# Kernel optimization log

Measured on AMD Instinct MI355X. Metric: run time of the kernel, lower is better.

## Reference

```python
import jax, jax.numpy as jnp
import numpy as np

B, T, D = 2, 2048, 2048
NH, NKV, HD = 16, 4, 128
EPS = 1e-6
ROPE_THETA = 10000.0


def rms_norm(x, w):
    # per-head RMSNorm over the last (head_dim) axis
    var = jnp.mean(jnp.square(x), axis=-1, keepdims=True)
    return x * jax.lax.rsqrt(var + EPS) * w


def rope_sin_cos(seq_len, dim, dtype):
    inv_freq = 1.0 / (ROPE_THETA ** (jnp.arange(0, dim, 2, dtype=jnp.float32) / dim))
    t = jnp.arange(seq_len, dtype=jnp.float32)
    ang = jnp.outer(t, inv_freq)                      # [T, HD/2]
    ang = jnp.concatenate([ang, ang], axis=-1)         # [T, HD]
    return jnp.sin(ang).astype(dtype), jnp.cos(ang).astype(dtype)


def rotate_half(x):
    x1, x2 = jnp.split(x, 2, axis=-1)
    return jnp.concatenate([-x2, x1], axis=-1)


def apply_rope(x, sin, cos):
    # x: [B, T, H, HD]; sin/cos: [T, HD]
    s = sin[None, :, None, :]
    c = cos[None, :, None, :]
    return x * c + rotate_half(x) * s


def setup_inputs() -> dict:
    key = jax.random.key(0)
    ks = jax.random.split(key, 5)
    scale = 1.0 / np.sqrt(D)
    return {
        "x": jax.random.normal(ks[0], (B, T, D), jnp.float32),
        "wq": jax.random.normal(ks[1], (D, D), jnp.float32) * scale,
        "wk": jax.random.normal(ks[2], (NKV * HD, D), jnp.float32) * scale,
        "wv": jax.random.normal(ks[3], (NKV * HD, D), jnp.float32) * scale,
        "wo": jax.random.normal(ks[4], (D, D), jnp.float32) * scale,
        "q_norm_w": jnp.ones((HD,), jnp.float32),
        "k_norm_w": jnp.ones((HD,), jnp.float32),
    }


def reference(x, wq, wk, wv, wo, q_norm_w, k_norm_w):
    b, t, _ = x.shape
    q = (x @ wq.T).reshape(b, t, NH, HD)    # [B,T,NH,HD]
    k = (x @ wk.T).reshape(b, t, NKV, HD)   # [B,T,NKV,HD]
    v = (x @ wv.T).reshape(b, t, NKV, HD)

    # per-head QK RMS norm
    q = rms_norm(q, q_norm_w)
    k = rms_norm(k, k_norm_w)

    # RoPE
    sin, cos = rope_sin_cos(t, HD, x.dtype)
    q = apply_rope(q, sin, cos)
    k = apply_rope(k, sin, cos)

    # GQA: expand kv heads to match query heads
    rep = NH // NKV
    k = jnp.repeat(k, rep, axis=2)          # [B,T,NH,HD]
    v = jnp.repeat(v, rep, axis=2)

    # causal SDPA
    scale = 1.0 / np.sqrt(HD)
    scores = jnp.einsum('bqhd,bkhd->bhqk', q, k) * scale
    causal = jnp.tril(jnp.ones((t, t), bool))
    scores = jnp.where(causal[None, None], scores, jnp.finfo(scores.dtype).min)
    probs = jax.nn.softmax(scores, axis=-1)
    att = jnp.einsum('bhqk,bkhd->bqhd', probs, v).reshape(b, t, NH * HD)
    return att @ wo.T
```

## Files before the change

kernel.cpp:

```cpp
#include <hip/hip_runtime.h>
#include <hip/hip_bf16.h>

#define B_ 2
#define T_ 2048
#define D_ 2048
#define NH_ 16
#define NKV_ 4
#define HD_ 128

using bf16 = __bf16;
using bf16x8 = __attribute__((ext_vector_type(8))) __bf16;
using bf16x4 = __attribute__((ext_vector_type(4))) __bf16;
using f32x4 = __attribute__((ext_vector_type(4))) float;

__device__ __forceinline__ void gld_lds16(bf16* lds, const bf16* g) {
  __builtin_amdgcn_global_load_lds(
      (const __attribute__((address_space(1))) void*)g,
      (__attribute__((address_space(3))) void*)lds, 16, 0, 0);
}

__global__ __launch_bounds__(256) void cvt_bf16(const float* __restrict__ in,
                                                bf16* __restrict__ out, int n4) {
  int i = blockIdx.x * 256 + threadIdx.x;
  if (i >= n4) return;
  float4 v = ((const float4*)in)[i];
  bf16x4 o;
  o[0] = (bf16)v.x; o[1] = (bf16)v.y; o[2] = (bf16)v.z; o[3] = (bf16)v.w;
  ((bf16x4*)out)[i] = o;
}

template<typename OutT>
__global__ __launch_bounds__(256) void gemm_bt(const bf16* __restrict__ A,
                                               const bf16* __restrict__ Bt,
                                               OutT* __restrict__ C,
                                               int M, int N, int K) {
  __shared__ bf16 As[128 * 32];
  __shared__ bf16 Bs[128 * 32];
  const int tid = threadIdx.x;
  const int wid = tid >> 6;
  const int lane = tid & 63;
  const int g = lane >> 4, r = lane & 15;
  const int wm = wid >> 1, wn = wid & 1;
  const int gx = gridDim.x;
  const int nwg = gx * gridDim.y;
  const int flat = blockIdx.y * gx + blockIdx.x;
  const int swz = (flat & 7) * (nwg >> 3) + (flat >> 3);
  const long bm = (long)(swz / gx) * 128, bn = (long)(swz % gx) * 128;
  f32x4 acc[4][4] = {};

  for (int k0 = 0; k0 < K; k0 += 32) {
    __syncthreads();
    for (int c = 0; c < 2; ++c) {
      int ch = wid * 2 + c;
      int row = ch * 16 + (lane >> 2);
      int col = (lane & 3) * 8;
      gld_lds16(As + ch * 512, A + (bm + row) * K + k0 + col);
      gld_lds16(Bs + ch * 512, Bt + (bn + row) * K + k0 + col);
    }
    asm volatile("s_waitcnt vmcnt(0)" ::: "memory");
    __syncthreads();
    bf16x8 af[4], bfr[4];
    for (int m = 0; m < 4; ++m)
      af[m] = *(const bf16x8*)(As + (wm * 64 + m * 16 + r) * 32 + g * 8);
    for (int n = 0; n < 4; ++n)
      bfr[n] = *(const bf16x8*)(Bs + (wn * 64 + n * 16 + r) * 32 + g * 8);
    for (int m = 0; m < 4; ++m)
      for (int n = 0; n < 4; ++n)
        acc[m][n] = __builtin_amdgcn_mfma_f32_16x16x32_bf16(af[m], bfr[n], acc[m][n], 0, 0, 0);
  }

  for (int m = 0; m < 4; ++m)
    for (int n = 0; n < 4; ++n)
      for (int e = 0; e < 4; ++e) {
        long row = bm + wm * 64 + m * 16 + g * 4 + e;
        long col = bn + wn * 64 + n * 16 + r;
        C[row * N + col] = (OutT)acc[m][n][e];
      }
}

template<int IS_K>
__global__ __launch_bounds__(256) void norm_rope(const bf16* __restrict__ qkv,
                                                 const float* __restrict__ w,
                                                 bf16* __restrict__ out) {
  const int lane = threadIdx.x & 63;
  const int rloc = threadIdx.x >> 6;
  const int NHH = IS_K ? NKV_ : NH_;
  const int COFF = IS_K ? 2048 : 0;
  const long rid = (long)blockIdx.x * 4 + rloc;
  const int h = (int)(rid % NHH);
  const long bt = rid / NHH;
  const int t = (int)(bt % T_);
  const bf16* src = qkv + bt * 3072 + COFF + h * HD_;
  float v0 = (float)src[lane];
  float v1 = (float)src[lane + 64];
  float ss = v0 * v0 + v1 * v1;
  for (int o = 1; o < 64; o <<= 1) ss += __shfl_xor(ss, o, 64);
  float inv = rsqrtf(ss * (1.f / HD_) + 1e-6f);
  float n0 = v0 * inv * w[lane];
  float n1 = v1 * inv * w[lane + 64];
  float ang = (float)t * exp2f((float)lane * (-13.287712379549449f / 64.f));
  float sv, cv;
  __sincosf(ang, &sv, &cv);
  float o0 = n0 * cv - n1 * sv;
  float o1 = n1 * cv + n0 * sv;
  bf16* dst;
  if (IS_K) {
    long b = bt / T_;
    dst = out + ((b * NKV_ + h) * (long)T_ + t) * HD_;
  } else {
    dst = out + (bt * NH_ + h) * HD_;
  }
  dst[lane] = (bf16)o0;
  dst[lane + 64] = (bf16)o1;
}

__global__ __launch_bounds__(256) void vpack(const bf16* __restrict__ qkv,
                                             bf16* __restrict__ Vt) {
  __shared__ float tile[64][65];
  const int tt = blockIdx.x;
  const int dd = blockIdx.y & 1;
  const int bkv = blockIdx.y >> 1;
  const long b = bkv >> 2;
  const int kv = bkv & 3;
  const int t0 = tt * 64, d0 = dd * 64;
  for (int i = 0; i < 2; ++i) {
    int row = i * 32 + (threadIdx.x >> 3);
    int c8 = (threadIdx.x & 7) * 8;
    bf16x8 v = *(const bf16x8*)&qkv[(b * T_ + t0 + row) * 3072 + 2560 + kv * HD_ + d0 + c8];
    for (int j = 0; j < 8; ++j) tile[row][c8 + j] = (float)v[j];
  }
  __syncthreads();
  for (int i = 0; i < 2; ++i) {
    int drow = i * 32 + (threadIdx.x >> 3);
    int tc8 = (threadIdx.x & 7) * 8;
    bf16x8 o;
    for (int j = 0; j < 8; ++j) o[j] = (bf16)tile[tc8 + j][drow];
    *(bf16x8*)&Vt[((b * NKV_ + kv) * (long)HD_ + d0 + drow) * T_ + t0 + tc8] = o;
  }
}

__global__ __launch_bounds__(512) void flash_attn(const bf16* __restrict__ Q,
                                                  const bf16* __restrict__ K,
                                                  const bf16* __restrict__ V,
                                                  bf16* __restrict__ O) {
  __shared__ bf16 Ks[2][64 * 128];
  __shared__ bf16 Vs[2][128 * 64];
  __shared__ bf16 Ps[8][16 * 64];
  const int h = blockIdx.y, b = blockIdx.z;
  const int qt = b ? blockIdx.x : (gridDim.x - 1) - blockIdx.x;
  const int kv = h >> 2;
  const int tid = threadIdx.x, wid = tid >> 6, lane = tid & 63;
  const int g = lane >> 4, r = lane & 15;
  const int q0 = qt * 128;
  const int qbase = q0 + wid * 16;
  const int q = qbase + r;

  bf16x8 aq[4];
  const bf16* qp = Q + ((long)(b * T_ + q)) * (NH_ * HD_) + h * HD_;
  for (int kk = 0; kk < 4; ++kk) aq[kk] = *(const bf16x8*)(qp + kk * 32 + g * 8);

  f32x4 oacc[8] = {};
  float m_run = -1e30f, l_run = 0.f;

  const bf16* Kbase = K + ((long)(b * NKV_ + kv)) * T_ * HD_;
  const bf16* Vbase = V + ((long)(b * NKV_ + kv)) * (long)HD_ * T_;
  const int nkt = 2 * qt + 2;

  auto stageKV = [&](int buf, int k0) {
    for (int c = 0; c < 2; ++c) {
      int ch = wid * 2 + c;
      {
        int row = ch * 4 + (lane >> 4);
        int srccol = ((lane & 15) ^ (row & 7)) * 8;
        gld_lds16(&Ks[buf][ch * 512], Kbase + (long)(k0 + row) * HD_ + srccol);
      }
      {
        int row = ch * 8 + (lane >> 3);
        int srccol = ((lane & 7) ^ (row & 7)) * 8;
        gld_lds16(&Vs[buf][ch * 512], Vbase + (long)row * T_ + k0 + srccol);
      }
    }
  };

  stageKV(0, 0);
  for (int kt = 0; kt < nkt; ++kt) {
    const int k0 = kt * 64;
    const int cur = kt & 1;
    if (kt + 1 < nkt) {
      stageKV(cur ^ 1, k0 + 64);
      asm volatile("s_waitcnt vmcnt(4)" ::: "memory");
    } else {
      asm volatile("s_waitcnt vmcnt(0)" ::: "memory");
    }
    __builtin_amdgcn_s_barrier();

    f32x4 s[4] = {};
    __builtin_amdgcn_s_setprio(1);
    for (int n = 0; n < 4; ++n)
      for (int kk = 0; kk < 4; ++kk) {
        int row = n * 16 + r;
        bf16x8 bk = *(const bf16x8*)(&Ks[cur][row * 128 + (((kk * 4 + g) ^ (row & 7)) * 8)]);
        s[n] = __builtin_amdgcn_mfma_f32_16x16x32_bf16(bk, aq[kk], s[n], 0, 0, 0);
      }
    __builtin_amdgcn_s_setprio(0);

    const float scale = 0.088388347648318447f;
    const bool domask = (k0 + 63 > qbase);
    float mx = -1e30f;
    if (domask) {
      for (int n = 0; n < 4; ++n) {
        const int km = k0 + n * 16 + g * 4;
        for (int e = 0; e < 4; ++e) {
          float v = s[n][e] * scale;
          if (km + e > q) v = -1e30f;
          s[n][e] = v;
          mx = fmaxf(mx, v);
        }
      }
    } else {
      for (int n = 0; n < 4; ++n)
        for (int e = 0; e < 4; ++e) {
          float v = s[n][e] * scale;
          s[n][e] = v;
          mx = fmaxf(mx, v);
        }
    }
    mx = fmaxf(mx, __shfl_xor(mx, 16, 64));
    mx = fmaxf(mx, __shfl_xor(mx, 32, 64));
    float mnew = fmaxf(m_run, mx);
    float alpha = __expf(m_run - mnew);
    float ls = 0.f;
    for (int n = 0; n < 4; ++n) {
      bf16x4 pb;
      for (int e = 0; e < 4; ++e) {
        float p = __expf(s[n][e] - mnew);
        ls += p;
        pb[e] = (bf16)p;
      }
      int c = n * 2 + (g >> 1);
      *(bf16x4*)(&Ps[wid][r * 64 + ((c ^ (r & 7)) * 8) + (g & 1) * 4]) = pb;
    }
    ls += __shfl_xor(ls, 16, 64);
    ls += __shfl_xor(ls, 32, 64);
    m_run = mnew;
    l_run = l_run * alpha + ls;

    float al[4];
    for (int e = 0; e < 4; ++e)
      al[e] = __shfl(alpha, (lane & 48) | (g * 4 + e), 64);
    for (int dt = 0; dt < 8; ++dt)
      for (int e = 0; e < 4; ++e) oacc[dt][e] *= al[e];

    asm volatile("s_waitcnt lgkmcnt(0)" ::: "memory");

    __builtin_amdgcn_s_setprio(1);
    for (int kk = 0; kk < 2; ++kk) {
      bf16x8 ap = *(const bf16x8*)(&Ps[wid][r * 64 + (((kk * 4 + g) ^ (r & 7)) * 8)]);
      for (int dt = 0; dt < 8; ++dt) {
        int row = dt * 16 + r;
        bf16x8 bv = *(const bf16x8*)(&Vs[cur][row * 64 + (((kk * 4 + g) ^ (row & 7)) * 8)]);
        oacc[dt] = __builtin_amdgcn_mfma_f32_16x16x32_bf16(ap, bv, oacc[dt], 0, 0, 0);
      }
    }
    __builtin_amdgcn_s_setprio(0);
    __builtin_amdgcn_s_barrier();
  }

  float li[4];
  for (int e = 0; e < 4; ++e) {
    float lv = __shfl(l_run, (lane & 48) | (g * 4 + e), 64);
    li[e] = 1.f / lv;
  }
  for (int e = 0; e < 4; ++e) {
    const int grow = q0 + wid * 16 + g * 4 + e;
    bf16* dst = O + ((long)(b * T_ + grow)) * (NH_ * HD_) + h * HD_;
    for (int dt = 0; dt < 8; ++dt)
      dst[dt * 16 + r] = (bf16)(oacc[dt][e] * li[e]);
  }
}

extern "C" void kernel_launch(void* const* d_in, const int* in_sizes, int n_in,
                              void* d_out, int out_size, void* d_ws, size_t ws_size,
                              hipStream_t stream) {
  const float* x  = (const float*)d_in[0];
  const float* wq = (const float*)d_in[1];
  const float* wk = (const float*)d_in[2];
  const float* wv = (const float*)d_in[3];
  const float* wo = (const float*)d_in[4];
  const float* qw = (const float*)d_in[5];
  const float* kw = (const float*)d_in[6];
  float* out = (float*)d_out;

  char* p = (char*)d_ws;
  bf16* xb    = (bf16*)(p);
  bf16* wqkvb = (bf16*)(p + 16777216);
  bf16* wob   = (bf16*)(p + 29360128);
  bf16* QKVr  = (bf16*)(p + 37748736);
  bf16* Qb    = (bf16*)(p + 62914560);
  bf16* Kb    = (bf16*)(p + 79691776);
  bf16* Vt    = (bf16*)(p + 83886080);
  bf16* attb  = (bf16*)(p + 88080384);

  cvt_bf16<<<8192, 256, 0, stream>>>(x,  xb, 2097152);
  cvt_bf16<<<4096, 256, 0, stream>>>(wq, wqkvb,           1048576);
  cvt_bf16<<<1024, 256, 0, stream>>>(wk, wqkvb + 4194304,  262144);
  cvt_bf16<<<1024, 256, 0, stream>>>(wv, wqkvb + 5242880,  262144);
  cvt_bf16<<<4096, 256, 0, stream>>>(wo, wob, 1048576);

  gemm_bt<bf16><<<dim3(24, 32), 256, 0, stream>>>(xb, wqkvb, QKVr, 4096, 3072, 2048);

  norm_rope<0><<<16384, 256, 0, stream>>>(QKVr, qw, Qb);
  norm_rope<1><<<4096, 256, 0, stream>>>(QKVr, kw, Kb);
  vpack<<<dim3(32, 16), 256, 0, stream>>>(QKVr, Vt);

  flash_attn<<<dim3(16, 16, 2), 512, 0, stream>>>(Qb, Kb, Vt, attb);

  gemm_bt<float><<<dim3(16, 32), 256, 0, stream>>>(attb, wob, out, 4096, 2048, 2048);
}
```

Baseline: 234.2 us.

## Triple-buffer GEMM LDS loads and fuse fp32-to-bf16 conversion launches

The GEMM main loop now uses three LDS buffers with asynchronous global-to-LDS loads issued two tiles ahead, waiting only on the oldest batch. This overlaps memory latency with MFMA work and replaces the two barriers per K step with one. Separately, the five conversion kernels are merged into a single launch that picks its source by block index, which cuts launch overhead. The triple buffer triples the LDS footprint (48 KB per block), which may lower occupancy.

```diff
diff --git a/kernel.cpp b/kernel.cpp
--- a/kernel.cpp
+++ b/kernel.cpp
@@ -19,14 +19,28 @@
       (__attribute__((address_space(3))) void*)lds, 16, 0, 0);
 }
 
-__global__ __launch_bounds__(256) void cvt_bf16(const float* __restrict__ in,
-                                                bf16* __restrict__ out, int n4) {
-  int i = blockIdx.x * 256 + threadIdx.x;
-  if (i >= n4) return;
-  float4 v = ((const float4*)in)[i];
+__global__ __launch_bounds__(256) void cvt_all(const float* __restrict__ x,
+                                               const float* __restrict__ wq,
+                                               const float* __restrict__ wk,
+                                               const float* __restrict__ wv,
+                                               const float* __restrict__ wo,
+                                               bf16* __restrict__ xb,
+                                               bf16* __restrict__ wqkvb,
+                                               bf16* __restrict__ wob) {
+  const int bid = blockIdx.x;
+  const float* src;
+  bf16* dst;
+  int base;
+  if (bid < 8192)       { src = x;  dst = xb;              base = bid; }
+  else if (bid < 12288) { src = wq; dst = wqkvb;           base = bid - 8192; }
+  else if (bid < 13312) { src = wk; dst = wqkvb + 4194304; base = bid - 12288; }
+  else if (bid < 14336) { src = wv; dst = wqkvb + 5242880; base = bid - 13312; }
+  else                  { src = wo; dst = wob;             base = bid - 14336; }
+  const int i = base * 256 + threadIdx.x;
+  float4 v = ((const float4*)src)[i];
   bf16x4 o;
   o[0] = (bf16)v.x; o[1] = (bf16)v.y; o[2] = (bf16)v.z; o[3] = (bf16)v.w;
-  ((bf16x4*)out)[i] = o;
+  ((bf16x4*)dst)[i] = o;
 }
 
 template<typename OutT>
@@ -34,8 +48,8 @@
                                                const bf16* __restrict__ Bt,
                                                OutT* __restrict__ C,
                                                int M, int N, int K) {
-  __shared__ bf16 As[128 * 32];
-  __shared__ bf16 Bs[128 * 32];
+  __shared__ bf16 As[3][128 * 32];
+  __shared__ bf16 Bs[3][128 * 32];
   const int tid = threadIdx.x;
   const int wid = tid >> 6;
   const int lane = tid & 63;
@@ -47,23 +61,34 @@
   const int swz = (flat & 7) * (nwg >> 3) + (flat >> 3);
   const long bm = (long)(swz / gx) * 128, bn = (long)(swz % gx) * 128;
   f32x4 acc[4][4] = {};
-
-  for (int k0 = 0; k0 < K; k0 += 32) {
-    __syncthreads();
+  const int NT = K >> 5;
+
+  auto stage = [&](int buf, int k0) {
     for (int c = 0; c < 2; ++c) {
       int ch = wid * 2 + c;
       int row = ch * 16 + (lane >> 2);
       int col = (lane & 3) * 8;
-      gld_lds16(As + ch * 512, A + (bm + row) * K + k0 + col);
-      gld_lds16(Bs + ch * 512, Bt + (bn + row) * K + k0 + col);
-    }
-    asm volatile("s_waitcnt vmcnt(0)" ::: "memory");
-    __syncthreads();
+      gld_lds16(&As[buf][ch * 512], A + (bm + row) * K + k0 + col);
+      gld_lds16(&Bs[buf][ch * 512], Bt + (bn + row) * K + k0 + col);
+    }
+  };
+
+  stage(0, 0);
+  stage(1, 32);
+  for (int t = 0; t < NT; ++t) {
+    if (t + 1 < NT)
+      asm volatile("s_waitcnt vmcnt(4)" ::: "memory");
+    else
+      asm volatile("s_waitcnt vmcnt(0)" ::: "memory");
+    __builtin_amdgcn_s_barrier();
+    if (t + 2 < NT) stage((t + 2) % 3, (t + 2) * 32);
+    const bf16* as = As[t % 3];
+    const bf16* bs = Bs[t % 3];
     bf16x8 af[4], bfr[4];
     for (int m = 0; m < 4; ++m)
-      af[m] = *(const bf16x8*)(As + (wm * 64 + m * 16 + r) * 32 + g * 8);
+      af[m] = *(const bf16x8*)(as + (wm * 64 + m * 16 + r) * 32 + g * 8);
     for (int n = 0; n < 4; ++n)
-      bfr[n] = *(const bf16x8*)(Bs + (wn * 64 + n * 16 + r) * 32 + g * 8);
+      bfr[n] = *(const bf16x8*)(bs + (wn * 64 + n * 16 + r) * 32 + g * 8);
     for (int m = 0; m < 4; ++m)
       for (int n = 0; n < 4; ++n)
         acc[m][n] = __builtin_amdgcn_mfma_f32_16x16x32_bf16(af[m], bfr[n], acc[m][n], 0, 0, 0);
@@ -301,11 +326,7 @@
   bf16* Vt    = (bf16*)(p + 83886080);
   bf16* attb  = (bf16*)(p + 88080384);
 
-  cvt_bf16<<<8192, 256, 0, stream>>>(x,  xb, 2097152);
-  cvt_bf16<<<4096, 256, 0, stream>>>(wq, wqkvb,           1048576);
-  cvt_bf16<<<1024, 256, 0, stream>>>(wk, wqkvb + 4194304,  262144);
-  cvt_bf16<<<1024, 256, 0, stream>>>(wv, wqkvb + 5242880,  262144);
-  cvt_bf16<<<4096, 256, 0, stream>>>(wo, wob, 1048576);
+  cvt_all<<<18432, 256, 0, stream>>>(x, wq, wk, wv, wo, xb, wqkvb, wob);
 
   gemm_bt<bf16><<<dim3(24, 32), 256, 0, stream>>>(xb, wqkvb, QKVr, 4096, 3072, 2048);
 
```

New measurement: 218.0 us. 6.9% less time.
